# Kernel optimization log

Measured on AMD Instinct MI355X. Metric: run time of the kernel, lower is better.

The kernel has to match this reference:

```python
import jax, jax.numpy as jnp
import numpy as np

MUL = 128          # shared multiplicity 'u' appended to all operands
DIM_IN = 4         # SO3 '0+1' -> 1 + 3 components
DIM_OUT = 4        # SO3 '0+1'
BATCH = 32768
NPATH = (2, 5, 12)  # coupling paths ('w' dim) for degree 1,2,3
BLOCK_ID = np.array([0, 1, 1, 1])  # irrep block of each of the 4 components


def setup_inputs() -> dict:
    key = jax.random.key(0)
    ks = jax.random.split(key, 8)
    x = jax.random.normal(ks[0], (BATCH, DIM_IN * MUL), jnp.float32)
    # one (mul,mul) channel-mixing matrix per irrep block, per degree (3 Linears)
    lin_w = jax.random.normal(ks[1], (3, 2, MUL, MUL), jnp.float32)
    # per-degree path weights, shape (num_paths, mul)
    w1 = jax.random.normal(ks[2], (NPATH[0], MUL), jnp.float32)
    w2 = jax.random.normal(ks[3], (NPATH[1], MUL), jnp.float32)
    w3 = jax.random.normal(ks[4], (NPATH[2], MUL), jnp.float32)
    # basis (Clebsch-Gordan-like) coefficient tensors C[a1..av, i, w], normalized
    C1 = jax.random.normal(ks[5], (DIM_IN, DIM_OUT, NPATH[0]), jnp.float32) / np.sqrt(DIM_IN * NPATH[0])
    C2 = jax.random.normal(ks[6], (DIM_IN, DIM_IN, DIM_OUT, NPATH[1]), jnp.float32) / np.sqrt(DIM_IN**2 * NPATH[1])
    C3 = jax.random.normal(ks[7], (DIM_IN, DIM_IN, DIM_IN, DIM_OUT, NPATH[2]), jnp.float32) / np.sqrt(DIM_IN**3 * NPATH[2])
    return {"x": x, "lin_w": lin_w, "w1": w1, "w2": w2, "w3": w3,
            "C1": C1, "C2": C2, "C3": C3}


def _linear(x3, w_deg):
    # x3: (n, dim, u); w_deg: (n_blocks=2, u, u). Per-irrep channel mixing.
    Wd = w_deg[BLOCK_ID]  # (dim, u, u) gathered per component
    return jnp.einsum('ndu,duv->ndv', x3, Wd) / np.sqrt(MUL)


def reference(x, lin_w, w1, w2, w3, C1, C2, C3):
    n = x.shape[0]
    x3 = x.reshape(n, DIM_IN, MUL)  # ir_mul layout: (component, channel)
    y1 = _linear(x3, lin_w[0])
    y2 = _linear(x3, lin_w[1])
    y3 = _linear(x3, lin_w[2])

    # degree 1: out += sum_{a,w} C1[a,i,w] w1[w,u] y1[n,a,u]
    C1u = jnp.einsum('aiw,wu->aiu', C1, w1)
    out = jnp.einsum('aiu,nau->niu', C1u, y1)

    # degree 2
    C2u = jnp.einsum('abiw,wu->abiu', C2, w2)
    T2 = jnp.einsum('abiu,nau->nbiu', C2u, y1)
    out = out + jnp.einsum('nbiu,nbu->niu', T2, y2)

    # degree 3 (staged to keep intermediates at (n, d, d, u) / (n, d, i, u))
    C3u = jnp.einsum('abciw,wu->abciu', C3, w3)
    G = jnp.einsum('nau,nbu->nabu', y1, y2)
    H = jnp.einsum('abciu,nabu->nciu', C3u, G)
    out = out + jnp.einsum('nciu,ncu->niu', H, y3)

    return out.reshape(n, DIM_OUT * MUL)
```

## Files before the change

kernel.cpp:

```cpp
#include <hip/hip_runtime.h>

typedef __attribute__((ext_vector_type(4))) float    f32x4;
typedef __attribute__((ext_vector_type(4))) short    s16x4;
typedef __attribute__((ext_vector_type(8))) short    s16x8;
typedef __attribute__((ext_vector_type(8))) _Float16 h16x8;

#define ROWS 16
#define XS_STRIDE 520

__device__ __forceinline__ short f2bf(float f) {
  unsigned u = __float_as_uint(f);
  u = (u + 0x7fffu + ((u >> 16) & 1u)) >> 16;
  return (short)u;
}

__global__ void precompute_kernel(const float* __restrict__ lin_w,
                                  const float* __restrict__ w1,
                                  const float* __restrict__ w2,
                                  const float* __restrict__ w3,
                                  const float* __restrict__ C1,
                                  const float* __restrict__ C2,
                                  const float* __restrict__ C3,
                                  short*    __restrict__ wF,
                                  _Float16* __restrict__ cc,
                                  float*    __restrict__ cu1) {
  int tid = blockIdx.x * blockDim.x + threadIdx.x;
  int nth = gridDim.x * blockDim.x;
  const float rs = 0.088388347648318447f;
  for (int idx = tid; idx < 6 * 8 * 4 * 64 * 8; idx += nth) {
    int j  = idx & 7;
    int ln = (idx >> 3) & 63;
    int kt = (idx >> 9) & 3;
    int vt = (idx >> 11) & 7;
    int d2 = idx >> 14;
    int v  = vt * 16 + (ln & 15);
    int k  = kt * 32 + (ln >> 4) * 8 + j;
    wF[idx] = f2bf(lin_w[(d2 * 128 + k) * 128 + v] * rs);
  }
  for (int idx = tid; idx < 128 * 16 * 20; idx += nth) {
    int v  = idx / 320;
    int r  = idx - v * 320;
    int ab = r / 20;
    int j  = r - ab * 20;
    int a = ab >> 2, b = ab & 3;
    float s = 0.f;
    if (j < 16) {
      int c = j >> 2, i = j & 3;
      const float* p = C3 + (((a * 4 + b) * 4 + c) * 4 + i) * 12;
      #pragma unroll
      for (int w = 0; w < 12; ++w) s += p[w] * w3[w * 128 + v];
    } else {
      int i = j - 16;
      const float* p = C2 + ((a * 4 + b) * 4 + i) * 5;
      #pragma unroll
      for (int w = 0; w < 5; ++w) s += p[w] * w2[w * 128 + v];
    }
    int byte_in_row = (ab * 48 + j * 2) ^ ((v & 7) << 4);
    cc[v * 384 + (byte_in_row >> 1)] = (_Float16)s;
  }
  for (int idx = tid; idx < 128 * 16; idx += nth) {
    int v = idx >> 4;
    int ai = idx & 15;
    int a = ai >> 2, i = ai & 3;
    cu1[idx] = C1[(a * 4 + i) * 2 + 0] * w1[v] + C1[(a * 4 + i) * 2 + 1] * w1[128 + v];
  }
}

__launch_bounds__(512, 2)
__global__ void main_kernel(const float* __restrict__ x,
                            const short* __restrict__ wF,
                            const _Float16* __restrict__ cc,
                            const float* __restrict__ cu1,
                            float* __restrict__ out) {
  __shared__ short xs[ROWS * XS_STRIDE];
  __shared__ __align__(16) char ccl[98304];

  const int t    = threadIdx.x;
  const int lane = t & 63;
  const int wave = t >> 6;
  const int vl   = lane & 15;
  const int quad = lane >> 4;
  const int n0   = blockIdx.x * ROWS;
  const int v    = wave * 16 + vl;

  s16x8 bf_cur[4], bf_nxt[4];
  {
    const s16x8* w0 = (const s16x8*)wF + wave * 256 + lane;
    #pragma unroll
    for (int kt = 0; kt < 4; ++kt) bf_cur[kt] = w0[kt * 64];
  }
  f32x4 c1v[4];
  {
    const f32x4* cu1v = (const f32x4*)(cu1 + v * 16);
    #pragma unroll
    for (int q = 0; q < 4; ++q) c1v[q] = cu1v[q];
  }
  __builtin_amdgcn_sched_barrier(0);

  const float4* xsrc = (const float4*)(x + (size_t)n0 * 512);
  #pragma unroll
  for (int i2 = 0; i2 < 4; ++i2) {
    int f = i2 * 512 + t;
    float4 xv = xsrc[f];
    int row = f >> 7, c4 = f & 127;
    s16x4 pk;
    pk[0] = f2bf(xv.x); pk[1] = f2bf(xv.y); pk[2] = f2bf(xv.z); pk[3] = f2bf(xv.w);
    *(s16x4*)&xs[row * XS_STRIDE + c4 * 4] = pk;
  }

  {
    const f32x4* csrc = (const f32x4*)cc;
    f32x4*       cdst = (f32x4*)ccl;
    #pragma unroll
    for (int i = 0; i < 12; ++i) cdst[i * 512 + t] = csrc[i * 512 + t];
  }
  __syncthreads();

  float yreg[12][4];

  #pragma unroll
  for (int d2 = 0; d2 < 6; ++d2) {
    if (d2 < 5) {
      const s16x8* wsrc = (const s16x8*)wF + ((d2 + 1) * 8 + wave) * 256 + lane;
      #pragma unroll
      for (int kt = 0; kt < 4; ++kt) bf_nxt[kt] = wsrc[kt * 64];
    }
    __builtin_amdgcn_sched_barrier(0);
    const int d = d2 >> 1, blk = d2 & 1;
    const int a_begin = blk ? 1 : 0;
    const int a_end   = blk ? 4 : 1;
    #pragma unroll
    for (int a = a_begin; a < a_end; ++a) {
      f32x4 acc = {0.f, 0.f, 0.f, 0.f};
      #pragma unroll
      for (int kt = 0; kt < 4; ++kt) {
        s16x8 af = *(const s16x8*)&xs[vl * XS_STRIDE + a * 128 + kt * 32 + quad * 8];
        acc = __builtin_amdgcn_mfma_f32_16x16x32_bf16(af, bf_cur[kt], acc, 0, 0, 0);
      }
      const int da = d * 4 + a;
      #pragma unroll
      for (int r = 0; r < 4; ++r) yreg[da][r] = acc[r];
    }
    #pragma unroll
    for (int kt = 0; kt < 4; ++kt) bf_cur[kt] = bf_nxt[kt];
  }

  float acc[4][4];

  {
    float c1[16];
    #pragma unroll
    for (int q = 0; q < 4; ++q) {
      c1[4 * q + 0] = c1v[q][0]; c1[4 * q + 1] = c1v[q][1];
      c1[4 * q + 2] = c1v[q][2]; c1[4 * q + 3] = c1v[q][3];
    }
    #pragma unroll
    for (int i = 0; i < 4; ++i)
      #pragma unroll
      for (int r = 0; r < 4; ++r) {
        float s = c1[0 * 4 + i] * yreg[0][r];
        s = fmaf(c1[1 * 4 + i], yreg[1][r], s);
        s = fmaf(c1[2 * 4 + i], yreg[2][r], s);
        s = fmaf(c1[3 * 4 + i], yreg[3][r], s);
        acc[i][r] = s;
      }
  }

  const char* myc = ccl + v * 768;
  const int   vm  = (v & 7) << 4;
  #pragma unroll
  for (int ab = 0; ab < 16; ++ab) {
    h16x8 h0 = *(const h16x8*)(myc + ((ab * 48 +  0) ^ vm));
    h16x8 h1 = *(const h16x8*)(myc + ((ab * 48 + 16) ^ vm));
    h16x8 h2 = *(const h16x8*)(myc + ((ab * 48 + 32) ^ vm));
    const int a = ab >> 2, b = ab & 3;
    float cj[20];
    #pragma unroll
    for (int j = 0; j < 8; ++j) { cj[j] = (float)h0[j]; cj[8 + j] = (float)h1[j]; }
    #pragma unroll
    for (int j = 0; j < 4; ++j) cj[16 + j] = (float)h2[j];
    #pragma unroll
    for (int r = 0; r < 4; ++r) {
      const float G = yreg[a][r] * yreg[4 + b][r];
      #pragma unroll
      for (int i = 0; i < 4; ++i) {
        float s = cj[16 + i];
        s = fmaf(cj[0 + i],  yreg[8][r],  s);
        s = fmaf(cj[4 + i],  yreg[9][r],  s);
        s = fmaf(cj[8 + i],  yreg[10][r], s);
        s = fmaf(cj[12 + i], yreg[11][r], s);
        acc[i][r] = fmaf(G, s, acc[i][r]);
      }
    }
  }

  #pragma unroll
  for (int r = 0; r < 4; ++r) {
    const int n = n0 + quad * 4 + r;
    #pragma unroll
    for (int i = 0; i < 4; ++i) out[(size_t)n * 512 + i * 128 + v] = acc[i][r];
  }
}

extern "C" void kernel_launch(void* const* d_in, const int* in_sizes, int n_in,
                              void* d_out, int out_size, void* d_ws, size_t ws_size,
                              hipStream_t stream) {
  const float* x     = (const float*)d_in[0];
  const float* lin_w = (const float*)d_in[1];
  const float* w1    = (const float*)d_in[2];
  const float* w2    = (const float*)d_in[3];
  const float* w3    = (const float*)d_in[4];
  const float* C1    = (const float*)d_in[5];
  const float* C2    = (const float*)d_in[6];
  const float* C3    = (const float*)d_in[7];

  char* ws = (char*)d_ws;
  short*    wF  = (short*)ws;
  _Float16* cc  = (_Float16*)(ws + 196608);
  float*    cu1 = (float*)(ws + 294912);
  float*    out = (float*)d_out;

  hipLaunchKernelGGL(precompute_kernel, dim3(384), dim3(256), 0, stream,
                     lin_w, w1, w2, w3, C1, C2, C3, wF, cc, cu1);
  hipLaunchKernelGGL(main_kernel, dim3(2048), dim3(512), 0, stream,
                     x, wF, cc, cu1, out);
}
```

Before: 185.4 us.

## Make main kernel persistent over 8 row tiles with double-buffered x prefetch

The main kernel now launches 256 blocks, and each one loops over 8 row tiles instead of handling a single tile. The 96KB coefficient table is copied into shared memory once per block, not once per tile. All six weight fragments are held in registers for the whole block. The next tile's x is prefetched into registers and written to a second shared buffer while the current tile computes. The risks are higher register pressure from 24 s16x8 weight registers plus the prefetch registers, and only 256 blocks to spread across the GPU's compute units.

```diff
diff --git a/kernel.cpp b/kernel.cpp
--- a/kernel.cpp
+++ b/kernel.cpp
@@ -7,6 +7,7 @@
 
 #define ROWS 16
 #define XS_STRIDE 520
+#define NTILE 8
 
 __device__ __forceinline__ short f2bf(float f) {
   unsigned u = __float_as_uint(f);
@@ -72,7 +73,7 @@
                             const _Float16* __restrict__ cc,
                             const float* __restrict__ cu1,
                             float* __restrict__ out) {
-  __shared__ short xs[ROWS * XS_STRIDE];
+  __shared__ short xs[2][ROWS * XS_STRIDE];
   __shared__ __align__(16) char ccl[98304];
 
   const int t    = threadIdx.x;
@@ -80,14 +81,15 @@
   const int wave = t >> 6;
   const int vl   = lane & 15;
   const int quad = lane >> 4;
-  const int n0   = blockIdx.x * ROWS;
+  const int b    = blockIdx.x;
   const int v    = wave * 16 + vl;
 
-  s16x8 bf_cur[4], bf_nxt[4];
-  {
-    const s16x8* w0 = (const s16x8*)wF + wave * 256 + lane;
-    #pragma unroll
-    for (int kt = 0; kt < 4; ++kt) bf_cur[kt] = w0[kt * 64];
+  s16x8 wreg[6][4];
+  #pragma unroll
+  for (int d2 = 0; d2 < 6; ++d2) {
+    const s16x8* wsrc = (const s16x8*)wF + (d2 * 8 + wave) * 256 + lane;
+    #pragma unroll
+    for (int kt = 0; kt < 4; ++kt) wreg[d2][kt] = wsrc[kt * 64];
   }
   f32x4 c1v[4];
   {
@@ -95,110 +97,126 @@
     #pragma unroll
     for (int q = 0; q < 4; ++q) c1v[q] = cu1v[q];
   }
-  __builtin_amdgcn_sched_barrier(0);
-
-  const float4* xsrc = (const float4*)(x + (size_t)n0 * 512);
-  #pragma unroll
-  for (int i2 = 0; i2 < 4; ++i2) {
-    int f = i2 * 512 + t;
-    float4 xv = xsrc[f];
-    int row = f >> 7, c4 = f & 127;
-    s16x4 pk;
-    pk[0] = f2bf(xv.x); pk[1] = f2bf(xv.y); pk[2] = f2bf(xv.z); pk[3] = f2bf(xv.w);
-    *(s16x4*)&xs[row * XS_STRIDE + c4 * 4] = pk;
-  }
-
   {
     const f32x4* csrc = (const f32x4*)cc;
     f32x4*       cdst = (f32x4*)ccl;
     #pragma unroll
     for (int i = 0; i < 12; ++i) cdst[i * 512 + t] = csrc[i * 512 + t];
   }
+  {
+    const float4* xsrc = (const float4*)(x + (size_t)b * ROWS * 512);
+    #pragma unroll
+    for (int i2 = 0; i2 < 4; ++i2) {
+      int f = i2 * 512 + t;
+      float4 xv = xsrc[f];
+      int row = f >> 7, c4 = f & 127;
+      s16x4 pk;
+      pk[0] = f2bf(xv.x); pk[1] = f2bf(xv.y); pk[2] = f2bf(xv.z); pk[3] = f2bf(xv.w);
+      *(s16x4*)&xs[0][row * XS_STRIDE + c4 * 4] = pk;
+    }
+  }
   __syncthreads();
 
-  float yreg[12][4];
-
-  #pragma unroll
-  for (int d2 = 0; d2 < 6; ++d2) {
-    if (d2 < 5) {
-      const s16x8* wsrc = (const s16x8*)wF + ((d2 + 1) * 8 + wave) * 256 + lane;
-      #pragma unroll
-      for (int kt = 0; kt < 4; ++kt) bf_nxt[kt] = wsrc[kt * 64];
+  float4 xp[4];
+  #pragma unroll 1
+  for (int k = 0; k < NTILE; ++k) {
+    const int cur = k & 1;
+    const int n0  = (k * 256 + b) * ROWS;
+
+    if (k + 1 < NTILE) {
+      const float4* xsrc = (const float4*)(x + (size_t)((k + 1) * 256 + b) * ROWS * 512);
+      #pragma unroll
+      for (int i2 = 0; i2 < 4; ++i2) xp[i2] = xsrc[i2 * 512 + t];
     }
     __builtin_amdgcn_sched_barrier(0);
-    const int d = d2 >> 1, blk = d2 & 1;
-    const int a_begin = blk ? 1 : 0;
-    const int a_end   = blk ? 4 : 1;
-    #pragma unroll
-    for (int a = a_begin; a < a_end; ++a) {
-      f32x4 acc = {0.f, 0.f, 0.f, 0.f};
-      #pragma unroll
-      for (int kt = 0; kt < 4; ++kt) {
-        s16x8 af = *(const s16x8*)&xs[vl * XS_STRIDE + a * 128 + kt * 32 + quad * 8];
-        acc = __builtin_amdgcn_mfma_f32_16x16x32_bf16(af, bf_cur[kt], acc, 0, 0, 0);
-      }
-      const int da = d * 4 + a;
-      #pragma unroll
-      for (int r = 0; r < 4; ++r) yreg[da][r] = acc[r];
-    }
-    #pragma unroll
-    for (int kt = 0; kt < 4; ++kt) bf_cur[kt] = bf_nxt[kt];
-  }
-
-  float acc[4][4];
-
-  {
-    float c1[16];
-    #pragma unroll
-    for (int q = 0; q < 4; ++q) {
-      c1[4 * q + 0] = c1v[q][0]; c1[4 * q + 1] = c1v[q][1];
-      c1[4 * q + 2] = c1v[q][2]; c1[4 * q + 3] = c1v[q][3];
-    }
-    #pragma unroll
-    for (int i = 0; i < 4; ++i)
+
+    float yreg[12][4];
+    #pragma unroll
+    for (int d2 = 0; d2 < 6; ++d2) {
+      const int d = d2 >> 1, blk = d2 & 1;
+      const int a_begin = blk ? 1 : 0;
+      const int a_end   = blk ? 4 : 1;
+      #pragma unroll
+      for (int a = a_begin; a < a_end; ++a) {
+        f32x4 acc4 = {0.f, 0.f, 0.f, 0.f};
+        #pragma unroll
+        for (int kt = 0; kt < 4; ++kt) {
+          s16x8 af = *(const s16x8*)&xs[cur][vl * XS_STRIDE + a * 128 + kt * 32 + quad * 8];
+          acc4 = __builtin_amdgcn_mfma_f32_16x16x32_bf16(af, wreg[d2][kt], acc4, 0, 0, 0);
+        }
+        const int da = d * 4 + a;
+        #pragma unroll
+        for (int r = 0; r < 4; ++r) yreg[da][r] = acc4[r];
+      }
+    }
+
+    float acc[4][4];
+    {
+      float c1[16];
+      #pragma unroll
+      for (int q = 0; q < 4; ++q) {
+        c1[4 * q + 0] = c1v[q][0]; c1[4 * q + 1] = c1v[q][1];
+        c1[4 * q + 2] = c1v[q][2]; c1[4 * q + 3] = c1v[q][3];
+      }
+      #pragma unroll
+      for (int i = 0; i < 4; ++i)
+        #pragma unroll
+        for (int r = 0; r < 4; ++r) {
+          float s = c1[0 * 4 + i] * yreg[0][r];
+          s = fmaf(c1[1 * 4 + i], yreg[1][r], s);
+          s = fmaf(c1[2 * 4 + i], yreg[2][r], s);
+          s = fmaf(c1[3 * 4 + i], yreg[3][r], s);
+          acc[i][r] = s;
+        }
+    }
+
+    const char* myc = ccl + v * 768;
+    const int   vm  = (v & 7) << 4;
+    #pragma unroll
+    for (int ab = 0; ab < 16; ++ab) {
+      h16x8 h0 = *(const h16x8*)(myc + ((ab * 48 +  0) ^ vm));
+      h16x8 h1 = *(const h16x8*)(myc + ((ab * 48 + 16) ^ vm));
+      h16x8 h2 = *(const h16x8*)(myc + ((ab * 48 + 32) ^ vm));
+      const int a = ab >> 2, b2 = ab & 3;
+      float cj[20];
+      #pragma unroll
+      for (int j = 0; j < 8; ++j) { cj[j] = (float)h0[j]; cj[8 + j] = (float)h1[j]; }
+      #pragma unroll
+      for (int j = 0; j < 4; ++j) cj[16 + j] = (float)h2[j];
       #pragma unroll
       for (int r = 0; r < 4; ++r) {
-        float s = c1[0 * 4 + i] * yreg[0][r];
-        s = fmaf(c1[1 * 4 + i], yreg[1][r], s);
-        s = fmaf(c1[2 * 4 + i], yreg[2][r], s);
-        s = fmaf(c1[3 * 4 + i], yreg[3][r], s);
-        acc[i][r] = s;
-      }
-  }
-
-  const char* myc = ccl + v * 768;
-  const int   vm  = (v & 7) << 4;
-  #pragma unroll
-  for (int ab = 0; ab < 16; ++ab) {
-    h16x8 h0 = *(const h16x8*)(myc + ((ab * 48 +  0) ^ vm));
-    h16x8 h1 = *(const h16x8*)(myc + ((ab * 48 + 16) ^ vm));
-    h16x8 h2 = *(const h16x8*)(myc + ((ab * 48 + 32) ^ vm));
-    const int a = ab >> 2, b = ab & 3;
-    float cj[20];
-    #pragma unroll
-    for (int j = 0; j < 8; ++j) { cj[j] = (float)h0[j]; cj[8 + j] = (float)h1[j]; }
-    #pragma unroll
-    for (int j = 0; j < 4; ++j) cj[16 + j] = (float)h2[j];
+        const float G = yreg[a][r] * yreg[4 + b2][r];
+        #pragma unroll
+        for (int i = 0; i < 4; ++i) {
+          float s = cj[16 + i];
+          s = fmaf(cj[0 + i],  yreg[8][r],  s);
+          s = fmaf(cj[4 + i],  yreg[9][r],  s);
+          s = fmaf(cj[8 + i],  yreg[10][r], s);
+          s = fmaf(cj[12 + i], yreg[11][r], s);
+          acc[i][r] = fmaf(G, s, acc[i][r]);
+        }
+      }
+    }
+
     #pragma unroll
     for (int r = 0; r < 4; ++r) {
-      const float G = yreg[a][r] * yreg[4 + b][r];
-      #pragma unroll
-      for (int i = 0; i < 4; ++i) {
-        float s = cj[16 + i];
-        s = fmaf(cj[0 + i],  yreg[8][r],  s);
-        s = fmaf(cj[4 + i],  yreg[9][r],  s);
-        s = fmaf(cj[8 + i],  yreg[10][r], s);
-        s = fmaf(cj[12 + i], yreg[11][r], s);
-        acc[i][r] = fmaf(G, s, acc[i][r]);
-      }
-    }
-  }
-
-  #pragma unroll
-  for (int r = 0; r < 4; ++r) {
-    const int n = n0 + quad * 4 + r;
-    #pragma unroll
-    for (int i = 0; i < 4; ++i) out[(size_t)n * 512 + i * 128 + v] = acc[i][r];
+      const int n = n0 + quad * 4 + r;
+      #pragma unroll
+      for (int i = 0; i < 4; ++i) out[(size_t)n * 512 + i * 128 + v] = acc[i][r];
+    }
+
+    if (k + 1 < NTILE) {
+      #pragma unroll
+      for (int i2 = 0; i2 < 4; ++i2) {
+        int f = i2 * 512 + t;
+        int row = f >> 7, c4 = f & 127;
+        s16x4 pk;
+        pk[0] = f2bf(xp[i2].x); pk[1] = f2bf(xp[i2].y);
+        pk[2] = f2bf(xp[i2].z); pk[3] = f2bf(xp[i2].w);
+        *(s16x4*)&xs[1 - cur][row * XS_STRIDE + c4 * 4] = pk;
+      }
+    }
+    __syncthreads();
   }
 }
 
@@ -222,6 +240,6 @@
 
   hipLaunchKernelGGL(precompute_kernel, dim3(384), dim3(256), 0, stream,
                      lin_w, w1, w2, w3, C1, C2, C3, wF, cc, cu1);
-  hipLaunchKernelGGL(main_kernel, dim3(2048), dim3(512), 0, stream,
+  hipLaunchKernelGGL(main_kernel, dim3(256), dim3(512), 0, stream,
                      x, wF, cc, cu1, out);
 }
```

Measured after the change: 168.2 us. 9.3% less time.
